# Kernel optimization log

Hardware: AMD Instinct MI355X
Metric: run time of the kernel (lower is better)

## Reference

```python
import jax, jax.numpy as jnp
import numpy as np

D_MODEL = 384
N_HEAD = 6
HEAD_SIZE = 64
T_LEN = 256
BATCH = 128


def layernorm(x, g, b, eps=1e-5):
    mu = jnp.mean(x, axis=-1, keepdims=True)
    var = jnp.mean(jnp.square(x - mu), axis=-1, keepdims=True)
    return (x - mu) * jax.lax.rsqrt(var + eps) * g + b


def setup_inputs() -> dict:
    key = jax.random.key(0)
    ks = jax.random.split(key, 16)
    s = 0.02
    return {
        "x": jax.random.normal(ks[0], (BATCH, T_LEN, D_MODEL), jnp.float32),
        "Wq": jax.random.normal(ks[1], (N_HEAD, D_MODEL, HEAD_SIZE), jnp.float32) * s,
        "Wk": jax.random.normal(ks[2], (N_HEAD, D_MODEL, HEAD_SIZE), jnp.float32) * s,
        "Wv": jax.random.normal(ks[3], (N_HEAD, D_MODEL, HEAD_SIZE), jnp.float32) * s,
        "Wp": jax.random.normal(ks[4], (N_HEAD * HEAD_SIZE, D_MODEL), jnp.float32) * s,
        "bp": jnp.zeros((D_MODEL,), jnp.float32),
        "W1": jax.random.normal(ks[5], (D_MODEL, 4 * D_MODEL), jnp.float32) * s,
        "b1": jnp.zeros((4 * D_MODEL,), jnp.float32),
        "W2": jax.random.normal(ks[6], (4 * D_MODEL, D_MODEL), jnp.float32) * s,
        "b2": jnp.zeros((D_MODEL,), jnp.float32),
        "g1": jnp.ones((D_MODEL,), jnp.float32),
        "be1": jnp.zeros((D_MODEL,), jnp.float32),
        "g2": jnp.ones((D_MODEL,), jnp.float32),
        "be2": jnp.zeros((D_MODEL,), jnp.float32),
    }


def reference(x, Wq, Wk, Wv, Wp, bp, W1, b1, W2, b2, g1, be1, g2, be2):
    B, T, C = x.shape
    # --- pre-LN causal multi-head attention ---
    h = layernorm(x, g1, be1)
    q = jnp.einsum('btd,hde->bhte', h, Wq)  # [B,H,T,E]
    k = jnp.einsum('btd,hde->bhte', h, Wk)
    v = jnp.einsum('btd,hde->bhte', h, Wv)
    scores = jnp.einsum('bhte,bhse->bhts', q, k) / jnp.sqrt(jnp.float32(HEAD_SIZE))
    causal = jnp.tril(jnp.ones((T, T), bool))
    scores = jnp.where(causal, scores, jnp.float32(-jnp.inf))
    wei = jax.nn.softmax(scores, axis=-1)  # dropout = identity (eval)
    out = jnp.einsum('bhts,bhse->bhte', wei, v)
    out = out.transpose(0, 2, 1, 3).reshape(B, T, N_HEAD * HEAD_SIZE)  # head-concat
    x = x + out @ Wp + bp
    # --- pre-LN FFN ---
    h2 = layernorm(x, g2, be2)
    ff = jax.nn.relu(h2 @ W1 + b1) @ W2 + b2
    return x + ff
```

## Files before the change

kernel.cpp:

```cpp
#include <hip/hip_runtime.h>
#include <hip/hip_bf16.h>

#define D_MODEL 384
#define N_HEAD  6
#define HEAD    64
#define T_LEN   256
#define BATCH   128
#define MROWS   (BATCH * T_LEN)
#define FF      1536

typedef __bf16 bf16x8 __attribute__((ext_vector_type(8)));
typedef float  f32x4  __attribute__((ext_vector_type(4)));
typedef unsigned short us8 __attribute__((ext_vector_type(8)));
using bf16 = __hip_bfloat16;

__device__ inline f32x4 mfma16(bf16x8 a, bf16x8 b, f32x4 c) {
    return __builtin_amdgcn_mfma_f32_16x16x32_bf16(a, b, c, 0, 0, 0);
}

#define GLOAD_LDS16(g, l) __builtin_amdgcn_global_load_lds( \
    (const __attribute__((address_space(1))) unsigned int*)(g), \
    (__attribute__((address_space(3))) unsigned int*)(l), 16, 0, 0)

__global__ __launch_bounds__(256) void prep_w(
    const float* __restrict__ Wq, const float* __restrict__ Wk, const float* __restrict__ Wv,
    const float* __restrict__ Wp, const float* __restrict__ W1, const float* __restrict__ W2,
    bf16* __restrict__ Wqkv_t, bf16* __restrict__ Wp_t,
    bf16* __restrict__ W1_t,   bf16* __restrict__ W2_t)
{
    int i = blockIdx.x * 256 + threadIdx.x;
    if (i < 1152 * 384) {
        int cc = i / 384, d = i - cc * 384;
        const float* src = cc < 384 ? Wq : (cc < 768 ? Wk : Wv);
        int c = cc < 384 ? cc : (cc < 768 ? cc - 384 : cc - 768);
        int h = c >> 6, e = c & 63;
        Wqkv_t[i] = __float2bfloat16(src[(h * 384 + d) * 64 + e]);
    }
    if (i < 384 * 384) {
        int o = i / 384, d = i - o * 384;
        Wp_t[i] = __float2bfloat16(Wp[d * 384 + o]);
    }
    if (i < 1536 * 384) {
        int o = i / 384, d = i - o * 384;
        W1_t[i] = __float2bfloat16(W1[d * 1536 + o]);
        int o2 = i / 1536, d2 = i - o2 * 1536;
        W2_t[i] = __float2bfloat16(W2[d2 * 384 + o2]);
    }
}

__global__ __launch_bounds__(256) void ln_k(
    const float* __restrict__ xin, const float* __restrict__ gg,
    const float* __restrict__ bb, bf16* __restrict__ outb)
{
    int wid  = blockIdx.x * 4 + (threadIdx.x >> 6);
    int lane = threadIdx.x & 63;
    const float* xr = xin + (size_t)wid * 384;
    float v[6]; float s = 0.f;
#pragma unroll
    for (int i = 0; i < 6; ++i) { v[i] = xr[lane + i * 64]; s += v[i]; }
#pragma unroll
    for (int mk = 1; mk < 64; mk <<= 1) s += __shfl_xor(s, mk);
    float mu = s * (1.f / 384.f);
    float vs = 0.f;
#pragma unroll
    for (int i = 0; i < 6; ++i) { float d = v[i] - mu; vs += d * d; }
#pragma unroll
    for (int mk = 1; mk < 64; mk <<= 1) vs += __shfl_xor(vs, mk);
    float rs = rsqrtf(vs * (1.f / 384.f) + 1e-5f);
    bf16* orow = outb + (size_t)wid * 384;
#pragma unroll
    for (int i = 0; i < 6; ++i) {
        int c = lane + i * 64;
        orow[c] = __float2bfloat16((v[i] - mu) * rs * gg[c] + bb[c]);
    }
}

__global__ __launch_bounds__(256) void tr_v(
    const bf16* __restrict__ v, bf16* __restrict__ vT)
{
    __shared__ bf16 L[256][68];
    int bh = blockIdx.x;
    int tid = threadIdx.x;
    const bf16* src = v + (size_t)bh * T_LEN * HEAD + (size_t)tid * HEAD;
#pragma unroll
    for (int c = 0; c < 8; ++c)
        *(us8*)&L[tid][c * 8] = *(const us8*)&src[c * 8];
    __syncthreads();
    bf16* dst = vT + (size_t)bh * HEAD * T_LEN;
#pragma unroll
    for (int i = 0; i < 8; ++i) {
        int idx = tid + i * 256;
        int e = idx >> 5, tc = (idx & 31) * 8;
        bf16x8 pk;
#pragma unroll
        for (int j = 0; j < 8; ++j) pk[j] = *(__bf16*)&L[tc + j][e];
        *(bf16x8*)&dst[(size_t)e * T_LEN + tc] = pk;
    }
}

enum { EPI_QKV = 0, EPI_PROJ = 1, EPI_FFN1 = 2, EPI_FFN2 = 3 };

template<int EPI, int K, int NTN>
__global__ __launch_bounds__(512) void gemm8(
    const bf16* __restrict__ A, const bf16* __restrict__ Bt,
    const float* __restrict__ bias, const float* __restrict__ resid,
    float* __restrict__ outf,
    bf16* __restrict__ outq, bf16* __restrict__ outk, bf16* __restrict__ outv,
    bf16* __restrict__ outb)
{
    extern __shared__ char smem[];
    bf16* Albase = (bf16*)smem;
    bf16* Blbase = (bf16*)(smem + 65536);
    constexpr int NT = K / 64;
    constexpr int nwg = (MROWS / 256) * NTN;
    int bid = blockIdx.x;
    int wg = (bid & 7) * (nwg >> 3) + (bid >> 3);
    int mt = wg / NTN, nt = wg - mt * NTN;
    int m0 = mt * 256, n0 = nt * 192;
    int tid = threadIdx.x, lane = tid & 63, w = tid >> 6;
    int r = lane & 15, g = lane >> 4;
    int lr8 = lane >> 3, l7 = lane & 7;
    int csw = (l7 ^ lr8) << 3;
    int wm = (w >> 1) * 64, wn = (w & 1) * 96;
    int sb = g ^ l7;

    const bf16* Ag = A  + (size_t)(m0 + w * 32 + lr8) * K + csw;
    const bf16* Bg = Bt + (size_t)(n0 + w * 24 + lr8) * K + csw;
    const int AL0 = w * 32 * 64;
    const int BL0 = w * 24 * 64;

#define STAGE(tt, bb) do { \
    const bf16* a_ = Ag + (tt) * 64; \
    bf16* al_ = Albase + (bb) * 16384 + AL0; \
    _Pragma("unroll") for (int q_ = 0; q_ < 4; ++q_) \
        GLOAD_LDS16(a_ + (size_t)q_ * 8 * K, al_ + q_ * 8 * 64); \
    const bf16* b_ = Bg + (tt) * 64; \
    bf16* bl_ = Blbase + (bb) * 12288 + BL0; \
    _Pragma("unroll") for (int q_ = 0; q_ < 3; ++q_) \
        GLOAD_LDS16(b_ + (size_t)q_ * 8 * K, bl_ + q_ * 8 * 64); \
} while (0)

    f32x4 acc[4][6];
#pragma unroll
    for (int i = 0; i < 4; ++i)
#pragma unroll
        for (int j = 0; j < 6; ++j) acc[i][j] = (f32x4){0.f, 0.f, 0.f, 0.f};

    STAGE(0, 0);
    STAGE(1, 1);

#define ITER(tt, VM, DOSTAGE) do { \
    int bb_ = (tt) & 1; \
    asm volatile("s_waitcnt vmcnt(" #VM ")" ::: "memory"); \
    __builtin_amdgcn_s_barrier(); \
    __builtin_amdgcn_sched_barrier(0); \
    const bf16* Ar_ = Albase + bb_ * 16384; \
    const bf16* Br_ = Blbase + bb_ * 12288; \
    bf16x8 af[4][2], bfv[6][2]; \
    _Pragma("unroll") for (int mi = 0; mi < 4; ++mi) { \
        int row_ = (wm + mi * 16 + r) * 64; \
        _Pragma("unroll") for (int kk = 0; kk < 2; ++kk) \
            af[mi][kk] = *(const bf16x8*)&Ar_[row_ + ((sb ^ (kk * 4)) << 3)]; \
    } \
    _Pragma("unroll") for (int ni = 0; ni < 6; ++ni) { \
        int row_ = (wn + ni * 16 + r) * 64; \
        _Pragma("unroll") for (int kk = 0; kk < 2; ++kk) \
            bfv[ni][kk] = *(const bf16x8*)&Br_[row_ + ((sb ^ (kk * 4)) << 3)]; \
    } \
    asm volatile("s_waitcnt lgkmcnt(0)" ::: "memory"); \
    __builtin_amdgcn_sched_barrier(0); \
    __builtin_amdgcn_s_barrier(); \
    if (DOSTAGE) STAGE((tt) + 2, bb_); \
    __builtin_amdgcn_s_setprio(1); \
    _Pragma("unroll") for (int kk = 0; kk < 2; ++kk) \
      _Pragma("unroll") for (int mi = 0; mi < 4; ++mi) \
        _Pragma("unroll") for (int ni = 0; ni < 6; ++ni) \
            acc[mi][ni] = mfma16(af[mi][kk], bfv[ni][kk], acc[mi][ni]); \
    __builtin_amdgcn_s_setprio(0); \
} while (0)

#pragma unroll 1
    for (int t = 0; t < NT - 2; ++t) ITER(t, 7, true);
    ITER(NT - 2, 7, false);
    ITER(NT - 1, 0, false);
#undef ITER
#undef STAGE

#pragma unroll
    for (int ni = 0; ni < 6; ++ni) {
        int n = n0 + wn + ni * 16 + r;
        float bn = 0.f;
        if constexpr (EPI != EPI_QKV) bn = bias[n];
#pragma unroll
        for (int mi = 0; mi < 4; ++mi) {
#pragma unroll
            for (int j = 0; j < 4; ++j) {
                int m = m0 + wm + mi * 16 + (g << 2) + j;
                float v = acc[mi][ni][j];
                if constexpr (EPI == EPI_QKV) {
                    int b = m >> 8, t = m & 255;
                    bf16* dst; int c;
                    if (n < 384)      { dst = outq; c = n; }
                    else if (n < 768) { dst = outk; c = n - 384; }
                    else              { dst = outv; c = n - 768; }
                    int h = c >> 6, e = c & 63;
                    dst[((size_t)(b * N_HEAD + h) * T_LEN + t) * HEAD + e] = __float2bfloat16(v);
                } else if constexpr (EPI == EPI_PROJ || EPI == EPI_FFN2) {
                    outf[(size_t)m * 384 + n] = resid[(size_t)m * 384 + n] + v + bn;
                } else {
                    float z = v + bn; z = z > 0.f ? z : 0.f;
                    outb[(size_t)m * FF + n] = __float2bfloat16(z);
                }
            }
        }
    }
}

__global__ __launch_bounds__(256) void attn_k(
    const bf16* __restrict__ q, const bf16* __restrict__ k,
    const bf16* __restrict__ vT, bf16* __restrict__ att)
{
    __shared__ bf16 Ksm[64][64];
    __shared__ bf16 Vsm[64][64];
    __shared__ bf16 Psm[4][16][64];
    int bid = blockIdx.x;
    int qt = bid & 3, bh = bid >> 2;
    int q0 = qt * 64;
    int tid = threadIdx.x, lane = tid & 63, w = tid >> 6;
    int r = lane & 15, g = lane >> 4, ko = g << 3;
    int lr = lane >> 3, lc = (lane & 7) << 3;

    const bf16* qp = q + ((size_t)bh * T_LEN + q0 + w * 16) * HEAD;
    bf16x8 qf[2];
    qf[0] = *(const bf16x8*)&qp[r * HEAD + ko];
    qf[1] = *(const bf16x8*)&qp[r * HEAD + ko + 32];

    f32x4 o[4];
#pragma unroll
    for (int i = 0; i < 4; ++i) o[i] = (f32x4){0.f, 0.f, 0.f, 0.f};
    float mrow[4], lrow[4];
#pragma unroll
    for (int j = 0; j < 4; ++j) { mrow[j] = -3.0e38f; lrow[j] = 0.f; }

    for (int st = 0; st <= qt; ++st) {
        int s0 = st * 64;
#pragma unroll
        for (int s = 0; s < 2; ++s) {
            int row0 = w * 16 + s * 8;
            GLOAD_LDS16(k  + ((size_t)bh * T_LEN + s0 + row0 + lr) * HEAD + lc, &Ksm[row0][0]);
            GLOAD_LDS16(vT + ((size_t)bh * HEAD + row0 + lr) * T_LEN + s0 + lc, &Vsm[row0][0]);
        }
        __syncthreads();

        f32x4 s[4];
#pragma unroll
        for (int i = 0; i < 4; ++i) s[i] = (f32x4){0.f, 0.f, 0.f, 0.f};
#pragma unroll
        for (int kk = 0; kk < 2; ++kk) {
#pragma unroll
            for (int ni = 0; ni < 4; ++ni) {
                bf16x8 kf = *(const bf16x8*)&Ksm[ni * 16 + r][kk * 32 + ko];
                s[ni] = mfma16(qf[kk], kf, s[ni]);
            }
        }
        int qrow = q0 + w * 16 + (g << 2);
        float tmax[4], fsc[4], tsum[4];
#pragma unroll
        for (int j = 0; j < 4; ++j) {
            float mx = -3.0e38f;
#pragma unroll
            for (int ni = 0; ni < 4; ++ni) {
                int col = s0 + ni * 16 + r;
                float sv = (col <= qrow + j) ? s[ni][j] * 0.125f : -3.0e38f;
                s[ni][j] = sv;
                mx = fmaxf(mx, sv);
            }
            tmax[j] = mx;
        }
#pragma unroll
        for (int mk = 1; mk < 16; mk <<= 1)
#pragma unroll
            for (int j = 0; j < 4; ++j) tmax[j] = fmaxf(tmax[j], __shfl_xor(tmax[j], mk));
#pragma unroll
        for (int j = 0; j < 4; ++j) {
            float mnew = fmaxf(mrow[j], tmax[j]);
            fsc[j] = __expf(mrow[j] - mnew);
            mrow[j] = mnew;
            float ss = 0.f;
#pragma unroll
            for (int ni = 0; ni < 4; ++ni) {
                float p = __expf(s[ni][j] - mnew);
                s[ni][j] = p; ss += p;
            }
            tsum[j] = ss;
        }
#pragma unroll
        for (int mk = 1; mk < 16; mk <<= 1)
#pragma unroll
            for (int j = 0; j < 4; ++j) tsum[j] += __shfl_xor(tsum[j], mk);
#pragma unroll
        for (int j = 0; j < 4; ++j) lrow[j] = lrow[j] * fsc[j] + tsum[j];
#pragma unroll
        for (int ni = 0; ni < 4; ++ni)
#pragma unroll
            for (int j = 0; j < 4; ++j) o[ni][j] *= fsc[j];
#pragma unroll
        for (int ni = 0; ni < 4; ++ni)
#pragma unroll
            for (int j = 0; j < 4; ++j)
                Psm[w][(g << 2) + j][ni * 16 + r] = __float2bfloat16(s[ni][j]);
#pragma unroll
        for (int kk = 0; kk < 2; ++kk) {
            bf16x8 pf = *(const bf16x8*)&Psm[w][r][kk * 32 + ko];
#pragma unroll
            for (int ni = 0; ni < 4; ++ni) {
                bf16x8 vf = *(const bf16x8*)&Vsm[ni * 16 + r][kk * 32 + ko];
                o[ni] = mfma16(pf, vf, o[ni]);
            }
        }
        __syncthreads();
    }

    int b = bh / N_HEAD, h = bh % N_HEAD;
#pragma unroll
    for (int ni = 0; ni < 4; ++ni)
#pragma unroll
        for (int j = 0; j < 4; ++j) {
            int t = q0 + w * 16 + (g << 2) + j;
            int e = h * HEAD + ni * 16 + r;
            att[((size_t)b * T_LEN + t) * D_MODEL + e] = __float2bfloat16(o[ni][j] / lrow[j]);
        }
}

#define GEMM_SMEM 114688

extern "C" void kernel_launch(void* const* d_in, const int* in_sizes, int n_in,
                              void* d_out, int out_size, void* d_ws, size_t ws_size,
                              hipStream_t stream)
{
    const float* x   = (const float*)d_in[0];
    const float* Wq  = (const float*)d_in[1];
    const float* Wk  = (const float*)d_in[2];
    const float* Wv  = (const float*)d_in[3];
    const float* Wp  = (const float*)d_in[4];
    const float* bp  = (const float*)d_in[5];
    const float* W1  = (const float*)d_in[6];
    const float* b1  = (const float*)d_in[7];
    const float* W2  = (const float*)d_in[8];
    const float* b2  = (const float*)d_in[9];
    const float* g1  = (const float*)d_in[10];
    const float* be1 = (const float*)d_in[11];
    const float* g2  = (const float*)d_in[12];
    const float* be2 = (const float*)d_in[13];
    float* out = (float*)d_out;

    char* ws = (char*)d_ws;
    size_t off = 0;
    auto alloc = [&](size_t bytes) { void* p = ws + off; off += (bytes + 255) & ~(size_t)255; return p; };
    bf16* Wqkv_t = (bf16*)alloc((size_t)1152 * 384 * 2);
    bf16* Wp_t   = (bf16*)alloc((size_t)384 * 384 * 2);
    bf16* W1_t   = (bf16*)alloc((size_t)1536 * 384 * 2);
    bf16* W2_t   = (bf16*)alloc((size_t)384 * 1536 * 2);
    bf16* h      = (bf16*)alloc((size_t)MROWS * 384 * 2);
    bf16* qb     = (bf16*)alloc((size_t)MROWS * 384 * 2);
    bf16* kb     = (bf16*)alloc((size_t)MROWS * 384 * 2);
    bf16* vTb    = (bf16*)alloc((size_t)MROWS * 384 * 2);
    bf16* attb   = (bf16*)alloc((size_t)MROWS * 384 * 2);
    float* x1    = (float*)alloc((size_t)MROWS * 384 * 4);
    bf16* ff1    = qb;
    bf16* vb     = (bf16*)x1;

    hipFuncSetAttribute(reinterpret_cast<const void*>(&gemm8<EPI_QKV, 384, 6>),
                        hipFuncAttributeMaxDynamicSharedMemorySize, GEMM_SMEM);
    hipFuncSetAttribute(reinterpret_cast<const void*>(&gemm8<EPI_PROJ, 384, 2>),
                        hipFuncAttributeMaxDynamicSharedMemorySize, GEMM_SMEM);
    hipFuncSetAttribute(reinterpret_cast<const void*>(&gemm8<EPI_FFN1, 384, 8>),
                        hipFuncAttributeMaxDynamicSharedMemorySize, GEMM_SMEM);
    hipFuncSetAttribute(reinterpret_cast<const void*>(&gemm8<EPI_FFN2, 1536, 2>),
                        hipFuncAttributeMaxDynamicSharedMemorySize, GEMM_SMEM);

    prep_w<<<2304, 256, 0, stream>>>(Wq, Wk, Wv, Wp, W1, W2, Wqkv_t, Wp_t, W1_t, W2_t);
    ln_k<<<MROWS / 4, 256, 0, stream>>>(x, g1, be1, h);
    gemm8<EPI_QKV, 384, 6><<<768, 512, GEMM_SMEM, stream>>>(
        h, Wqkv_t, nullptr, nullptr, nullptr, qb, kb, vb, nullptr);
    tr_v<<<BATCH * N_HEAD, 256, 0, stream>>>(vb, vTb);
    attn_k<<<BATCH * N_HEAD * 4, 256, 0, stream>>>(qb, kb, vTb, attb);
    gemm8<EPI_PROJ, 384, 2><<<256, 512, GEMM_SMEM, stream>>>(
        attb, Wp_t, bp, x, x1, nullptr, nullptr, nullptr, nullptr);
    ln_k<<<MROWS / 4, 256, 0, stream>>>(x1, g2, be2, h);
    gemm8<EPI_FFN1, 384, 8><<<1024, 512, GEMM_SMEM, stream>>>(
        h, W1_t, b1, nullptr, nullptr, nullptr, nullptr, nullptr, ff1);
    gemm8<EPI_FFN2, 1536, 2><<<256, 512, GEMM_SMEM, stream>>>(
        ff1, W2_t, b2, x1, out, nullptr, nullptr, nullptr, nullptr);
}
```

Before: 294.7 us.

## Shrink GEMM M-tile, swap MFMA operands for vectorized epilogue, store fused QKV layout

The GEMM tile height drops from 256 to 128 rows, so LDS use falls to about 80KB and twice as many workgroups launch. Operand order in the MFMA is swapped so each lane holds four consecutive N columns, which lets the epilogue write vectorized 4-wide stores and load bias and residual as float4. The QKV projection now writes one interleaved [M,1152] buffer instead of scattering into per-head q/k/v tensors, and attention and the V transpose read from it with a 1152 stride. The change trades arithmetic intensity per tile for occupancy and coalesced writes, and it also reorders the LDS fragment loads to run per k-step.

```diff
diff --git a/kernel.cpp b/kernel.cpp
--- a/kernel.cpp
+++ b/kernel.cpp
@@ -12,6 +12,7 @@
 typedef __bf16 bf16x8 __attribute__((ext_vector_type(8)));
 typedef float  f32x4  __attribute__((ext_vector_type(4)));
 typedef unsigned short us8 __attribute__((ext_vector_type(8)));
+typedef unsigned short us4 __attribute__((ext_vector_type(4)));
 using bf16 = __hip_bfloat16;
 
 __device__ inline f32x4 mfma16(bf16x8 a, bf16x8 b, f32x4 c) {
@@ -76,12 +77,13 @@
 }
 
 __global__ __launch_bounds__(256) void tr_v(
-    const bf16* __restrict__ v, bf16* __restrict__ vT)
+    const bf16* __restrict__ qkv, bf16* __restrict__ vT)
 {
     __shared__ bf16 L[256][68];
     int bh = blockIdx.x;
+    int b = bh / N_HEAD, h = bh - b * N_HEAD;
     int tid = threadIdx.x;
-    const bf16* src = v + (size_t)bh * T_LEN * HEAD + (size_t)tid * HEAD;
+    const bf16* src = qkv + (size_t)(b * T_LEN + tid) * 1152 + 768 + h * 64;
 #pragma unroll
     for (int c = 0; c < 8; ++c)
         *(us8*)&L[tid][c * 8] = *(const us8*)&src[c * 8];
@@ -101,38 +103,36 @@
 enum { EPI_QKV = 0, EPI_PROJ = 1, EPI_FFN1 = 2, EPI_FFN2 = 3 };
 
 template<int EPI, int K, int NTN>
-__global__ __launch_bounds__(512) void gemm8(
+__global__ __launch_bounds__(512, 4) void gemm8(
     const bf16* __restrict__ A, const bf16* __restrict__ Bt,
     const float* __restrict__ bias, const float* __restrict__ resid,
-    float* __restrict__ outf,
-    bf16* __restrict__ outq, bf16* __restrict__ outk, bf16* __restrict__ outv,
-    bf16* __restrict__ outb)
+    float* __restrict__ outf, bf16* __restrict__ outq, bf16* __restrict__ outb)
 {
     extern __shared__ char smem[];
     bf16* Albase = (bf16*)smem;
-    bf16* Blbase = (bf16*)(smem + 65536);
+    bf16* Blbase = (bf16*)(smem + 32768);
     constexpr int NT = K / 64;
-    constexpr int nwg = (MROWS / 256) * NTN;
+    constexpr int nwg = (MROWS / 128) * NTN;
     int bid = blockIdx.x;
     int wg = (bid & 7) * (nwg >> 3) + (bid >> 3);
     int mt = wg / NTN, nt = wg - mt * NTN;
-    int m0 = mt * 256, n0 = nt * 192;
+    int m0 = mt * 128, n0 = nt * 192;
     int tid = threadIdx.x, lane = tid & 63, w = tid >> 6;
     int r = lane & 15, g = lane >> 4;
     int lr8 = lane >> 3, l7 = lane & 7;
     int csw = (l7 ^ lr8) << 3;
-    int wm = (w >> 1) * 64, wn = (w & 1) * 96;
+    int wm = (w & 3) * 32, wn = (w >> 2) * 96;
     int sb = g ^ l7;
 
-    const bf16* Ag = A  + (size_t)(m0 + w * 32 + lr8) * K + csw;
+    const bf16* Ag = A  + (size_t)(m0 + w * 16 + lr8) * K + csw;
     const bf16* Bg = Bt + (size_t)(n0 + w * 24 + lr8) * K + csw;
-    const int AL0 = w * 32 * 64;
+    const int AL0 = w * 16 * 64;
     const int BL0 = w * 24 * 64;
 
 #define STAGE(tt, bb) do { \
     const bf16* a_ = Ag + (tt) * 64; \
-    bf16* al_ = Albase + (bb) * 16384 + AL0; \
-    _Pragma("unroll") for (int q_ = 0; q_ < 4; ++q_) \
+    bf16* al_ = Albase + (bb) * 8192 + AL0; \
+    _Pragma("unroll") for (int q_ = 0; q_ < 2; ++q_) \
         GLOAD_LDS16(a_ + (size_t)q_ * 8 * K, al_ + q_ * 8 * 64); \
     const bf16* b_ = Bg + (tt) * 64; \
     bf16* bl_ = Blbase + (bb) * 12288 + BL0; \
@@ -140,100 +140,105 @@
         GLOAD_LDS16(b_ + (size_t)q_ * 8 * K, bl_ + q_ * 8 * 64); \
 } while (0)
 
-    f32x4 acc[4][6];
-#pragma unroll
-    for (int i = 0; i < 4; ++i)
+    f32x4 acc[2][6];
+#pragma unroll
+    for (int i = 0; i < 2; ++i)
 #pragma unroll
         for (int j = 0; j < 6; ++j) acc[i][j] = (f32x4){0.f, 0.f, 0.f, 0.f};
 
     STAGE(0, 0);
     STAGE(1, 1);
 
-#define ITER(tt, VM, DOSTAGE) do { \
+#define ITER(tt, VMS, DOSTAGE) do { \
     int bb_ = (tt) & 1; \
-    asm volatile("s_waitcnt vmcnt(" #VM ")" ::: "memory"); \
+    asm volatile("s_waitcnt vmcnt(" VMS ")" ::: "memory"); \
     __builtin_amdgcn_s_barrier(); \
     __builtin_amdgcn_sched_barrier(0); \
-    const bf16* Ar_ = Albase + bb_ * 16384; \
+    const bf16* Ar_ = Albase + bb_ * 8192; \
     const bf16* Br_ = Blbase + bb_ * 12288; \
-    bf16x8 af[4][2], bfv[6][2]; \
-    _Pragma("unroll") for (int mi = 0; mi < 4; ++mi) { \
-        int row_ = (wm + mi * 16 + r) * 64; \
-        _Pragma("unroll") for (int kk = 0; kk < 2; ++kk) \
-            af[mi][kk] = *(const bf16x8*)&Ar_[row_ + ((sb ^ (kk * 4)) << 3)]; \
+    _Pragma("unroll") for (int kk = 0; kk < 2; ++kk) { \
+        int so_ = (sb ^ (kk * 4)) << 3; \
+        bf16x8 af0 = *(const bf16x8*)&Ar_[(wm + r) * 64 + so_]; \
+        bf16x8 af1 = *(const bf16x8*)&Ar_[(wm + 16 + r) * 64 + so_]; \
+        bf16x8 bfv[6]; \
+        _Pragma("unroll") for (int ni = 0; ni < 6; ++ni) \
+            bfv[ni] = *(const bf16x8*)&Br_[(wn + ni * 16 + r) * 64 + so_]; \
+        asm volatile("s_waitcnt lgkmcnt(0)" ::: "memory"); \
+        __builtin_amdgcn_sched_barrier(0); \
+        __builtin_amdgcn_s_setprio(1); \
+        _Pragma("unroll") for (int ni = 0; ni < 6; ++ni) { \
+            acc[0][ni] = mfma16(bfv[ni], af0, acc[0][ni]); \
+            acc[1][ni] = mfma16(bfv[ni], af1, acc[1][ni]); \
+        } \
+        __builtin_amdgcn_s_setprio(0); \
     } \
-    _Pragma("unroll") for (int ni = 0; ni < 6; ++ni) { \
-        int row_ = (wn + ni * 16 + r) * 64; \
-        _Pragma("unroll") for (int kk = 0; kk < 2; ++kk) \
-            bfv[ni][kk] = *(const bf16x8*)&Br_[row_ + ((sb ^ (kk * 4)) << 3)]; \
-    } \
-    asm volatile("s_waitcnt lgkmcnt(0)" ::: "memory"); \
-    __builtin_amdgcn_sched_barrier(0); \
     __builtin_amdgcn_s_barrier(); \
     if (DOSTAGE) STAGE((tt) + 2, bb_); \
-    __builtin_amdgcn_s_setprio(1); \
-    _Pragma("unroll") for (int kk = 0; kk < 2; ++kk) \
-      _Pragma("unroll") for (int mi = 0; mi < 4; ++mi) \
-        _Pragma("unroll") for (int ni = 0; ni < 6; ++ni) \
-            acc[mi][ni] = mfma16(af[mi][kk], bfv[ni][kk], acc[mi][ni]); \
-    __builtin_amdgcn_s_setprio(0); \
 } while (0)
 
 #pragma unroll 1
-    for (int t = 0; t < NT - 2; ++t) ITER(t, 7, true);
-    ITER(NT - 2, 7, false);
-    ITER(NT - 1, 0, false);
+    for (int t = 0; t < NT - 2; ++t) ITER(t, "5", true);
+    ITER(NT - 2, "5", false);
+    ITER(NT - 1, "0", false);
 #undef ITER
 #undef STAGE
 
 #pragma unroll
-    for (int ni = 0; ni < 6; ++ni) {
-        int n = n0 + wn + ni * 16 + r;
-        float bn = 0.f;
-        if constexpr (EPI != EPI_QKV) bn = bias[n];
-#pragma unroll
-        for (int mi = 0; mi < 4; ++mi) {
-#pragma unroll
-            for (int j = 0; j < 4; ++j) {
-                int m = m0 + wm + mi * 16 + (g << 2) + j;
-                float v = acc[mi][ni][j];
-                if constexpr (EPI == EPI_QKV) {
-                    int b = m >> 8, t = m & 255;
-                    bf16* dst; int c;
-                    if (n < 384)      { dst = outq; c = n; }
-                    else if (n < 768) { dst = outk; c = n - 384; }
-                    else              { dst = outv; c = n - 768; }
-                    int h = c >> 6, e = c & 63;
-                    dst[((size_t)(b * N_HEAD + h) * T_LEN + t) * HEAD + e] = __float2bfloat16(v);
-                } else if constexpr (EPI == EPI_PROJ || EPI == EPI_FFN2) {
-                    outf[(size_t)m * 384 + n] = resid[(size_t)m * 384 + n] + v + bn;
-                } else {
-                    float z = v + bn; z = z > 0.f ? z : 0.f;
-                    outb[(size_t)m * FF + n] = __float2bfloat16(z);
+    for (int mi = 0; mi < 2; ++mi) {
+        size_t m = m0 + wm + mi * 16 + r;
+#pragma unroll
+        for (int ni = 0; ni < 6; ++ni) {
+            int nb = n0 + wn + ni * 16 + (g << 2);
+            f32x4 a = acc[mi][ni];
+            if constexpr (EPI == EPI_QKV) {
+                us4 u;
+#pragma unroll
+                for (int j = 0; j < 4; ++j) {
+                    __bf16 hb = (__bf16)a[j];
+                    u[j] = __builtin_bit_cast(unsigned short, hb);
                 }
+                *(us4*)&outq[m * 1152 + nb] = u;
+            } else if constexpr (EPI == EPI_FFN1) {
+                f32x4 b4 = *(const f32x4*)&bias[nb];
+                us4 u;
+#pragma unroll
+                for (int j = 0; j < 4; ++j) {
+                    float z = a[j] + b4[j]; z = z > 0.f ? z : 0.f;
+                    __bf16 hb = (__bf16)z;
+                    u[j] = __builtin_bit_cast(unsigned short, hb);
+                }
+                *(us4*)&outb[m * FF + nb] = u;
+            } else {
+                f32x4 b4 = *(const f32x4*)&bias[nb];
+                f32x4 rv = *(const f32x4*)&resid[m * 384 + nb];
+                f32x4 o;
+#pragma unroll
+                for (int j = 0; j < 4; ++j) o[j] = rv[j] + a[j] + b4[j];
+                *(f32x4*)&outf[m * 384 + nb] = o;
             }
         }
     }
 }
 
 __global__ __launch_bounds__(256) void attn_k(
-    const bf16* __restrict__ q, const bf16* __restrict__ k,
-    const bf16* __restrict__ vT, bf16* __restrict__ att)
+    const bf16* __restrict__ qkv, const bf16* __restrict__ vT,
+    bf16* __restrict__ att)
 {
     __shared__ bf16 Ksm[64][64];
     __shared__ bf16 Vsm[64][64];
     __shared__ bf16 Psm[4][16][64];
     int bid = blockIdx.x;
     int qt = bid & 3, bh = bid >> 2;
+    int b = bh / N_HEAD, h = bh - b * N_HEAD;
     int q0 = qt * 64;
     int tid = threadIdx.x, lane = tid & 63, w = tid >> 6;
     int r = lane & 15, g = lane >> 4, ko = g << 3;
     int lr = lane >> 3, lc = (lane & 7) << 3;
 
-    const bf16* qp = q + ((size_t)bh * T_LEN + q0 + w * 16) * HEAD;
+    const bf16* qbase = qkv + (size_t)b * T_LEN * 1152 + h * 64;
     bf16x8 qf[2];
-    qf[0] = *(const bf16x8*)&qp[r * HEAD + ko];
-    qf[1] = *(const bf16x8*)&qp[r * HEAD + ko + 32];
+    qf[0] = *(const bf16x8*)&qbase[(size_t)(q0 + w * 16 + r) * 1152 + ko];
+    qf[1] = *(const bf16x8*)&qbase[(size_t)(q0 + w * 16 + r) * 1152 + ko + 32];
 
     f32x4 o[4];
 #pragma unroll
@@ -247,7 +252,7 @@
 #pragma unroll
         for (int s = 0; s < 2; ++s) {
             int row0 = w * 16 + s * 8;
-            GLOAD_LDS16(k  + ((size_t)bh * T_LEN + s0 + row0 + lr) * HEAD + lc, &Ksm[row0][0]);
+            GLOAD_LDS16(qbase + (size_t)(s0 + row0 + lr) * 1152 + 384 + lc, &Ksm[row0][0]);
             GLOAD_LDS16(vT + ((size_t)bh * HEAD + row0 + lr) * T_LEN + s0 + lc, &Vsm[row0][0]);
         }
         __syncthreads();
@@ -321,7 +326,6 @@
         __syncthreads();
     }
 
-    int b = bh / N_HEAD, h = bh % N_HEAD;
 #pragma unroll
     for (int ni = 0; ni < 4; ++ni)
 #pragma unroll
@@ -332,7 +336,7 @@
         }
 }
 
-#define GEMM_SMEM 114688
+#define GEMM_SMEM 81920
 
 extern "C" void kernel_launch(void* const* d_in, const int* in_sizes, int n_in,
                               void* d_out, int out_size, void* d_ws, size_t ws_size,
@@ -362,13 +366,11 @@
     bf16* W1_t   = (bf16*)alloc((size_t)1536 * 384 * 2);
     bf16* W2_t   = (bf16*)alloc((size_t)384 * 1536 * 2);
     bf16* h      = (bf16*)alloc((size_t)MROWS * 384 * 2);
-    bf16* qb     = (bf16*)alloc((size_t)MROWS * 384 * 2);
-    bf16* kb     = (bf16*)alloc((size_t)MROWS * 384 * 2);
-    bf16* vTb    = (bf16*)alloc((size_t)MROWS * 384 * 2);
+    bf16* qkv    = (bf16*)alloc((size_t)MROWS * 1152 * 2);
     bf16* attb   = (bf16*)alloc((size_t)MROWS * 384 * 2);
     float* x1    = (float*)alloc((size_t)MROWS * 384 * 4);
-    bf16* ff1    = qb;
-    bf16* vb     = (bf16*)x1;
+    bf16* vTb    = h;
+    bf16* ff1    = qkv;
 
     hipFuncSetAttribute(reinterpret_cast<const void*>(&gemm8<EPI_QKV, 384, 6>),
                         hipFuncAttributeMaxDynamicSharedMemorySize, GEMM_SMEM);
@@ -381,15 +383,15 @@
 
     prep_w<<<2304, 256, 0, stream>>>(Wq, Wk, Wv, Wp, W1, W2, Wqkv_t, Wp_t, W1_t, W2_t);
     ln_k<<<MROWS / 4, 256, 0, stream>>>(x, g1, be1, h);
-    gemm8<EPI_QKV, 384, 6><<<768, 512, GEMM_SMEM, stream>>>(
-        h, Wqkv_t, nullptr, nullptr, nullptr, qb, kb, vb, nullptr);
-    tr_v<<<BATCH * N_HEAD, 256, 0, stream>>>(vb, vTb);
-    attn_k<<<BATCH * N_HEAD * 4, 256, 0, stream>>>(qb, kb, vTb, attb);
-    gemm8<EPI_PROJ, 384, 2><<<256, 512, GEMM_SMEM, stream>>>(
-        attb, Wp_t, bp, x, x1, nullptr, nullptr, nullptr, nullptr);
+    gemm8<EPI_QKV, 384, 6><<<1536, 512, GEMM_SMEM, stream>>>(
+        h, Wqkv_t, nullptr, nullptr, nullptr, qkv, nullptr);
+    tr_v<<<BATCH * N_HEAD, 256, 0, stream>>>(qkv, vTb);
+    attn_k<<<BATCH * N_HEAD * 4, 256, 0, stream>>>(qkv, vTb, attb);
+    gemm8<EPI_PROJ, 384, 2><<<512, 512, GEMM_SMEM, stream>>>(
+        attb, Wp_t, bp, x, x1, nullptr, nullptr);
     ln_k<<<MROWS / 4, 256, 0, stream>>>(x1, g2, be2, h);
-    gemm8<EPI_FFN1, 384, 8><<<1024, 512, GEMM_SMEM, stream>>>(
-        h, W1_t, b1, nullptr, nullptr, nullptr, nullptr, nullptr, ff1);
-    gemm8<EPI_FFN2, 1536, 2><<<256, 512, GEMM_SMEM, stream>>>(
-        ff1, W2_t, b2, x1, out, nullptr, nullptr, nullptr, nullptr);
-}
+    gemm8<EPI_FFN1, 384, 8><<<2048, 512, GEMM_SMEM, stream>>>(
+        h, W1_t, b1, nullptr, nullptr, nullptr, ff1);
+    gemm8<EPI_FFN2, 1536, 2><<<512, 512, GEMM_SMEM, stream>>>(
+        ff1, W2_t, b2, x1, out, nullptr, nullptr);
+}
```

New measurement: 307.2 us. +4.2%, slower.
